# Kernel tuning notes

Measured on AMD Instinct MI355X. Metric: run time of the kernel, lower is better.

## Reference

```python
import jax, jax.numpy as jnp
import numpy as np

N, M, NNZ, N_C, D = 4096, 4096, 262144, 4, 128
ADD_RATIO, TEMP = 0.1, 0.5


def setup_inputs() -> dict:
    key = jax.random.key(0)
    ks = jax.random.split(key, 6)
    X = jax.random.normal(ks[0], (N, D), dtype=jnp.float32)
    V = jax.random.randint(ks[1], (NNZ,), 0, N)
    E = jax.random.randint(ks[2], (NNZ,), 0, M)
    # incidence matrix consistent with the (V, E) pairs
    H = jnp.zeros((N, M), jnp.float32).at[V, E].set(1.0)
    incident_mask_prob = jax.random.uniform(ks[3], (N, M), jnp.float32, 1e-4, 1.0 - 1e-4)
    cos_weight = jax.random.normal(ks[4], (N_C, D), dtype=jnp.float32)
    eps = jax.random.uniform(ks[5], (N, M), jnp.float32, 1e-6, 1.0 - 1e-6)
    return {"X": X, "H": H, "V": V, "E": E,
            "incident_mask_prob": incident_mask_prob,
            "cos_weight": cos_weight, "eps": eps}


def _l2norm(x):
    # F.normalize(p=2, dim=-1): x / max(||x||, 1e-12)
    return x / jnp.maximum(jnp.linalg.norm(x, axis=-1, keepdims=True), 1e-12)


def reference(X, H, V, E, incident_mask_prob, cos_weight, eps):
    # scatter-mean of node embeddings into edge embeddings: eX [M, D]
    counts = jax.ops.segment_sum(jnp.ones((NNZ,), X.dtype), E, num_segments=M)
    eX = jax.ops.segment_sum(X[V], E, num_segments=M) / jnp.maximum(counts, 1.0)[:, None]

    node_fc = _l2norm(X[:, None, :] * cos_weight[None])   # [N, C, D]
    edge_fc = _l2norm(eX[:, None, :] * cos_weight[None])  # [M, C, D]
    # mean over C of per-channel cosine sims -> S [N, M]
    S = jnp.einsum('ncd,mcd->nm', node_fc, edge_fc) / N_C
    S = S.at[V, E].set(-1e30)  # mask existing incidences

    num_add = max(1, int(ADD_RATIO * NNZ))
    _, idx = jax.lax.top_k(S.reshape(-1), num_add)
    row = idx // M
    col = idx % M
    delta_H = jnp.zeros_like(H).at[row, col].set(1.0)
    enriched_H = H + delta_H

    # gumbel-sigmoid with straight-through estimator
    logit = (jnp.log(eps) - jnp.log(1.0 - eps)
             + jnp.log(incident_mask_prob + 1e-8)
             - jnp.log(1.0 - incident_mask_prob + 1e-8))
    soft = jax.nn.sigmoid(logit / TEMP)
    hard = (soft > 0.5).astype(soft.dtype)
    incident_mask = hard - jax.lax.stop_gradient(soft) + soft
    return enriched_H * incident_mask
```

## Files before the change

### kernel.cpp

```cpp
#include <hip/hip_runtime.h>

#define N_NODES 4096
#define M_EDGES 4096
#define NNZ_K   262144
#define NCH     4
#define DIM     128
#define KDIM    512
#define NM      (N_NODES * M_EDGES)
#define NUM_ADD 26214
#define NCB     2048
#define NFB     32768
#define CAP     262144
#define CAP2    65536

#define EXD_OFF   0ull
#define AFC_OFF   4194304ull
#define BFC_OFF   8388608ull
#define BKT_OFF   12582912ull
#define CVAL_OFF  13631488ull
#define CIDX_OFF  15728640ull
#define CIDX2_OFF 16777216ull
#define CNT_OFF   17039360ull
#define OFFS_OFF  17055744ull
#define CUR_OFF   17072132ull
#define HIST_OFF  17088516ull
#define FHIST_OFF 17096708ull
#define SCL_OFF   17227784ull
#define ZERO_BYTES (17227848ull - CNT_OFF)
#define NINV_OFF  17227904ull
#define EINV_OFF  17358976ull

typedef short bf16x8 __attribute__((ext_vector_type(8)));
typedef float f32x4  __attribute__((ext_vector_type(4)));

#define GLOAD_LDS16(gsrc, ldst)                                                 \
    __builtin_amdgcn_global_load_lds(                                           \
        (const __attribute__((address_space(1))) void*)(gsrc),                  \
        (__attribute__((address_space(3))) void*)(ldst), 16, 0, 0)

__device__ __forceinline__ int bin_c(float s) {
    int b = (int)floorf((s + 1.0f) * 1024.0f);
    return min(max(b, 0), NCB - 1);
}

__device__ __forceinline__ int fbin_of(double v, int bstar) {
    double lo = (double)(bstar - 12) * (2.0 / 2048.0) - 1.0;
    double wd = (28.0 * (2.0 / 2048.0)) / (double)NFB;
    int f = (int)floor((v - lo) / wd);
    return min(max(f, 0), NFB - 1);
}

__device__ __forceinline__ float hard_mask(float p, float e) {
    float logit = logf(e) - logf(1.0f - e) + logf(p + 1e-8f) - logf(1.0f - p + 1e-8f);
    float soft  = 1.0f / (1.0f + expf(-2.0f * logit));
    return (soft > 0.5f) ? 1.0f : 0.0f;
}

__device__ __forceinline__ unsigned short to_bf16_rtne(float f) {
    unsigned int b = __float_as_uint(f);
    b += 0x7FFFu + ((b >> 16) & 1u);
    return (unsigned short)(b >> 16);
}

__global__ void k_count(const int* __restrict__ E, int* __restrict__ cnt) {
    int k = blockIdx.x * 256 + threadIdx.x;
    if (k < NNZ_K) atomicAdd(&cnt[E[k]], 1);
}

__global__ __launch_bounds__(256) void k_scan(const int* __restrict__ cnt, int* __restrict__ offs) {
    __shared__ int part[256];
    int t = threadIdx.x;
    int loc[16]; int s = 0;
    for (int j = 0; j < 16; ++j) { loc[j] = cnt[t * 16 + j]; s += loc[j]; }
    part[t] = s;
    __syncthreads();
    if (t == 0) { int acc = 0; for (int i = 0; i < 256; ++i) { int v = part[i]; part[i] = acc; acc += v; } }
    __syncthreads();
    int acc = part[t];
    for (int j = 0; j < 16; ++j) { offs[t * 16 + j] = acc; acc += loc[j]; }
    if (t == 255) offs[4096] = acc;
}

__global__ void k_fill(const int* __restrict__ E, const int* __restrict__ offs,
                       int* __restrict__ cur, int* __restrict__ bkt) {
    int k = blockIdx.x * 256 + threadIdx.x;
    if (k < NNZ_K) {
        int e = E[k];
        int pos = atomicAdd(&cur[e], 1);
        bkt[offs[e] + pos] = k;
    }
}

__global__ __launch_bounds__(128) void k_edge_mean(
        const int* __restrict__ Vv, const int* __restrict__ cnt,
        const int* __restrict__ offs, const int* __restrict__ bkt,
        const float* __restrict__ X, double* __restrict__ eXd) {
    __shared__ int sk[1024];
    __shared__ int sv[1024];
    int m = blockIdx.x;
    int c = cnt[m]; if (c > 1024) c = 1024;
    int off = offs[m];
    for (int t = threadIdx.x; t < c; t += 128) sk[t] = bkt[off + t];
    __syncthreads();
    for (int t = threadIdx.x; t < c; t += 128) {
        int key = sk[t]; int r = 0;
        for (int j = 0; j < c; ++j) r += (sk[j] < key);
        sv[r] = Vv[key];
    }
    __syncthreads();
    int d = threadIdx.x;
    double s = 0.0;
    for (int j = 0; j < c; ++j) s += (double)X[sv[j] * DIM + d];
    eXd[m * DIM + d] = s / (double)(c > 1 ? c : 1);
}

template <typename T>
__global__ __launch_bounds__(128) void k_fc(const T* __restrict__ in,
                                            const float* __restrict__ w,
                                            unsigned short* __restrict__ out,
                                            double* __restrict__ dinv) {
    __shared__ double red[128];
    int n = blockIdx.x, d = threadIdx.x;
    double x = (double)in[n * DIM + d];
    for (int c = 0; c < NCH; ++c) {
        double v = x * (double)w[c * DIM + d];
        red[d] = v * v;
        __syncthreads();
        for (int s = 64; s > 0; s >>= 1) { if (d < s) red[d] += red[d + s]; __syncthreads(); }
        double denom = fmax(sqrt(red[0]), 1e-12);
        __syncthreads();
        out[n * KDIM + c * DIM + d] = to_bf16_rtne((float)(v / denom));
        if (d == 0) dinv[n * NCH + c] = 1.0 / denom;
    }
}

__global__ __launch_bounds__(256) void k_gemm_mfma(const unsigned short* __restrict__ A,
                                                   const unsigned short* __restrict__ B,
                                                   float* __restrict__ S) {
    __shared__ short As[128][32];
    __shared__ short Bs[128][32];
    int tid = threadIdx.x;
    int row0 = blockIdx.y * 128, col0 = blockIdx.x * 128;
    int w = tid >> 6, l = tid & 63;
    int wr = (w >> 1) * 64, wc = (w & 1) * 64;
    f32x4 acc[4][4] = {};
    int lrow = l >> 2, lcol = (l & 3) * 8;
    int rb0 = (w * 2 + 0) * 16, rb1 = (w * 2 + 1) * 16;
    const unsigned short* sA0 = A + (size_t)(row0 + rb0 + lrow) * KDIM + lcol;
    const unsigned short* sA1 = A + (size_t)(row0 + rb1 + lrow) * KDIM + lcol;
    const unsigned short* sB0 = B + (size_t)(col0 + rb0 + lrow) * KDIM + lcol;
    const unsigned short* sB1 = B + (size_t)(col0 + rb1 + lrow) * KDIM + lcol;
    for (int k0 = 0; k0 < KDIM; k0 += 32) {
        __syncthreads();
        GLOAD_LDS16(sA0 + k0, &As[rb0][0]);
        GLOAD_LDS16(sA1 + k0, &As[rb1][0]);
        GLOAD_LDS16(sB0 + k0, &Bs[rb0][0]);
        GLOAD_LDS16(sB1 + k0, &Bs[rb1][0]);
        __syncthreads();
        int kq = (l >> 4) * 8;
        bf16x8 af[4], bfr[4];
        #pragma unroll
        for (int m = 0; m < 4; ++m) af[m] = *(const bf16x8*)&As[wr + m * 16 + (l & 15)][kq];
        #pragma unroll
        for (int n = 0; n < 4; ++n) bfr[n] = *(const bf16x8*)&Bs[wc + n * 16 + (l & 15)][kq];
        #pragma unroll
        for (int m = 0; m < 4; ++m)
            #pragma unroll
            for (int n = 0; n < 4; ++n)
                acc[m][n] = __builtin_amdgcn_mfma_f32_16x16x32_bf16(af[m], bfr[n], acc[m][n], 0, 0, 0);
    }
    #pragma unroll
    for (int m = 0; m < 4; ++m) {
        int r = row0 + wr + m * 16 + (l >> 4) * 4;
        #pragma unroll
        for (int n = 0; n < 4; ++n) {
            int c = col0 + wc + n * 16 + (l & 15);
            #pragma unroll
            for (int j = 0; j < 4; ++j)
                S[(size_t)(r + j) * M_EDGES + c] = 0.25f * acc[m][n][j];
        }
    }
}

__global__ void k_mask(const int* __restrict__ Vv, const int* __restrict__ E,
                       float* __restrict__ S) {
    int k = blockIdx.x * 256 + threadIdx.x;
    if (k < NNZ_K) S[(size_t)Vv[k] * M_EDGES + E[k]] = -1e30f;
}

__global__ __launch_bounds__(256) void k_hist_coarse(const float4* __restrict__ S4,
                                                     int* __restrict__ hist) {
    __shared__ int h[4][NCB + 8];
    int t = threadIdx.x;
    for (int i = t; i < 4 * (NCB + 8); i += 256) ((int*)h)[i] = 0;
    __syncthreads();
    int* hc = h[t & 3];
    int stride = gridDim.x * 256;
    for (int i = blockIdx.x * 256 + t; i < NM / 4; i += stride) {
        float4 v = S4[i];
        if (v.x > -2.0f) atomicAdd(&hc[bin_c(v.x)], 1);
        if (v.y > -2.0f) atomicAdd(&hc[bin_c(v.y)], 1);
        if (v.z > -2.0f) atomicAdd(&hc[bin_c(v.z)], 1);
        if (v.w > -2.0f) atomicAdd(&hc[bin_c(v.w)], 1);
    }
    __syncthreads();
    for (int i = t; i < NCB; i += 256) {
        int s = h[0][i] + h[1][i] + h[2][i] + h[3][i];
        if (s) atomicAdd(&hist[i], s);
    }
}

__global__ __launch_bounds__(256) void k_findcut(const int* __restrict__ hist, int* __restrict__ scl) {
    __shared__ int part[256];
    __shared__ int sb;
    int t = threadIdx.x;
    int loc[8]; int s = 0;
    for (int j = 0; j < 8; ++j) { loc[j] = hist[t * 8 + j]; s += loc[j]; }
    part[t] = s;
    __syncthreads();
    if (t == 0) { int acc = 0; for (int i = 255; i >= 0; --i) { int v = part[i]; part[i] = acc; acc += v; } }
    __syncthreads();
    int run = part[t];
    for (int j = 7; j >= 0; --j) {
        int h = loc[j];
        run += h;
        if (run >= NUM_ADD && run - h < NUM_ADD) { scl[0] = t * 8 + j; sb = t * 8 + j; }
    }
    __syncthreads();
    int bstar = sb;
    int g = 0;
    for (int i = bstar + 11 + t; i < NCB; i += 256) g += hist[i];
    part[t] = g;
    __syncthreads();
    for (int st2 = 128; st2 > 0; st2 >>= 1) { if (t < st2) part[t] += part[t + st2]; __syncthreads(); }
    if (t == 0) scl[1] = part[0];
}

__global__ __launch_bounds__(256) void k_collect(const float4* __restrict__ S4,
        int* __restrict__ scl, int* __restrict__ cidx, int* __restrict__ cidx2) {
    __shared__ unsigned short buf1[4096];
    __shared__ unsigned short buf2[4096];
    __shared__ int c1, c2;
    __shared__ unsigned long long gbase;
    int t = threadIdx.x;
    if (t == 0) { c1 = 0; c2 = 0; }
    __syncthreads();
    int bstar = scl[0];
    size_t base4 = (size_t)blockIdx.x * 1024 + t;
    float4 v0 = S4[base4];
    float4 v1 = S4[base4 + 256];
    float4 v2 = S4[base4 + 512];
    float4 v3 = S4[base4 + 768];
    #define COLLECT1(sc, loc)                                                   \
        if ((sc) > -2.0f) {                                                     \
            int b = bin_c(sc);                                                  \
            if (b >= bstar + 11)      buf2[atomicAdd(&c2, 1)] = (unsigned short)(loc); \
            else if (b >= bstar - 11) buf1[atomicAdd(&c1, 1)] = (unsigned short)(loc); \
        }
    #define COLLECT4(v, q)                                                      \
        COLLECT1((v).x, (t + (q)*256) * 4 + 0) COLLECT1((v).y, (t + (q)*256) * 4 + 1) \
        COLLECT1((v).z, (t + (q)*256) * 4 + 2) COLLECT1((v).w, (t + (q)*256) * 4 + 3)
    COLLECT4(v0, 0) COLLECT4(v1, 1) COLLECT4(v2, 2) COLLECT4(v3, 3)
    #undef COLLECT4
    #undef COLLECT1
    __syncthreads();
    if (t == 0) {
        unsigned long long pack = (unsigned long long)(unsigned)c1
                                | ((unsigned long long)(unsigned)c2 << 32);
        gbase = atomicAdd((unsigned long long*)&scl[8], pack);
    }
    __syncthreads();
    int g1 = (int)(gbase & 0xffffffffull);
    int g2 = (int)(gbase >> 32);
    int gb = blockIdx.x * 4096;
    for (int j = t; j < c1; j += 256) { int g = g1 + j; if (g < CAP)  cidx[g]  = gb + buf1[j]; }
    for (int j = t; j < c2; j += 256) { int g = g2 + j; if (g < CAP2) cidx2[g] = gb + buf2[j]; }
}

__global__ void k_scatter(const int* __restrict__ Vv, const int* __restrict__ E,
                          const float* __restrict__ prob, const float* __restrict__ eps,
                          float* __restrict__ out) {
    int k = blockIdx.x * 256 + threadIdx.x;
    if (k < NNZ_K) {
        size_t idx = (size_t)Vv[k] * M_EDGES + E[k];
        out[idx] = hard_mask(prob[idx], eps[idx]);
    }
}

__global__ __launch_bounds__(256) void k_selc(const int* __restrict__ scl,
        const int* __restrict__ cidx2,
        const float* __restrict__ prob, const float* __restrict__ eps,
        float* __restrict__ out) {
    int n = scl[9]; if (n > CAP2) n = CAP2;
    for (int i = blockIdx.x * 256 + threadIdx.x; i < n; i += 256 * 128) {
        int idx = cidx2[i];
        out[idx] = hard_mask(prob[idx], eps[idx]);
    }
}

__global__ __launch_bounds__(256) void k_exact(
        const int* __restrict__ scl, const int* __restrict__ cidx, double* __restrict__ cval,
        const float* __restrict__ X, const double* __restrict__ eXd, const float* __restrict__ cw,
        const double* __restrict__ ninv, const double* __restrict__ einv) {
    int nc = scl[8]; if (nc > CAP) nc = CAP;
    int wid = (blockIdx.x * 256 + threadIdx.x) >> 6;
    int l = threadIdx.x & 63;
    int nw = gridDim.x * 4;
    double w2[NCH][2];
    #pragma unroll
    for (int c = 0; c < NCH; ++c) {
        float2 wc2 = *(const float2*)&cw[c * DIM + 2 * l];
        w2[c][0] = (double)wc2.x * (double)wc2.x;
        w2[c][1] = (double)wc2.y * (double)wc2.y;
    }
    for (int i = wid; i < nc; i += nw) {
        int idx = cidx[i];
        int n = idx >> 12, m = idx & (M_EDGES - 1);
        float2  x2 = *(const float2*)&X[n * DIM + 2 * l];
        double2 e2 = *(const double2*)&eXd[m * DIM + 2 * l];
        double p0 = (double)x2.x * e2.x;
        double p1 = (double)x2.y * e2.y;
        double dt0 = p0 * w2[0][0] + p1 * w2[0][1];
        double dt1 = p0 * w2[1][0] + p1 * w2[1][1];
        double dt2 = p0 * w2[2][0] + p1 * w2[2][1];
        double dt3 = p0 * w2[3][0] + p1 * w2[3][1];
        #pragma unroll
        for (int s = 1; s < 64; s <<= 1) {
            dt0 += __shfl_xor(dt0, s);
            dt1 += __shfl_xor(dt1, s);
            dt2 += __shfl_xor(dt2, s);
            dt3 += __shfl_xor(dt3, s);
        }
        if (l == 0) {
            const double* nv = &ninv[n * NCH];
            const double* ev = &einv[m * NCH];
            cval[i] = 0.25 * (dt0 * nv[0] * ev[0] + dt1 * nv[1] * ev[1]
                            + dt2 * nv[2] * ev[2] + dt3 * nv[3] * ev[3]);
        }
    }
}

__global__ __launch_bounds__(256) void k_fhist(const int* __restrict__ scl,
                                               const int* __restrict__ cidx,
                                               const double* __restrict__ cval,
                                               int* __restrict__ fh) {
    int nc = scl[8]; if (nc > CAP) nc = CAP;
    int bstar = scl[0];
    for (int i = blockIdx.x * 256 + threadIdx.x; i < nc; i += 256 * 256)
        atomicAdd(&fh[fbin_of(cval[i], bstar)], 1);
}

__global__ __launch_bounds__(1024) void k_ffind(const int* __restrict__ fh, int* __restrict__ scl) {
    __shared__ int part[1024];
    int T = NUM_ADD - scl[1];
    int t = threadIdx.x;
    int loc[32]; int s = 0;
    for (int j = 0; j < 32; ++j) { loc[j] = fh[t * 32 + j]; s += loc[j]; }
    part[t] = s;
    __syncthreads();
    if (t == 0) { int acc = 0; for (int i = 1023; i >= 0; --i) { int v = part[i]; part[i] = acc; acc += v; } }
    __syncthreads();
    int run = part[t];
    for (int j = 31; j >= 0; --j) {
        int h = loc[j];
        run += h;
        if (run >= T && run - h < T) { scl[4] = t * 32 + j; scl[5] = run - h; }
    }
}

__global__ __launch_bounds__(256) void k_write(
        const int* __restrict__ scl, const int* __restrict__ cidx, const double* __restrict__ cval,
        const float* __restrict__ prob, const float* __restrict__ eps,
        float* __restrict__ out) {
    int nc = scl[8]; if (nc > CAP) nc = CAP;
    int fs = scl[4], bstar = scl[0];
    for (int i = blockIdx.x * 256 + threadIdx.x; i < nc; i += 256 * 256) {
        if (fbin_of(cval[i], bstar) > fs) {
            int idx = cidx[i];
            out[idx] = hard_mask(prob[idx], eps[idx]);
        }
    }
}

__global__ __launch_bounds__(256) void k_tie(
        const int* __restrict__ scl, const int* __restrict__ cidx, const double* __restrict__ cval,
        const float* __restrict__ prob, const float* __restrict__ eps,
        float* __restrict__ out) {
    __shared__ double mv[256];
    __shared__ int    mi[256];
    __shared__ int    cnt;
    int nc = scl[8]; if (nc > CAP) nc = CAP;
    int T = NUM_ADD - scl[1];
    int fs = scl[4], G1f = scl[5], bstar = scl[0];
    int t = threadIdx.x;
    if (t == 0) cnt = 0;
    __syncthreads();
    for (int i = t; i < nc; i += 256) {
        if (fbin_of(cval[i], bstar) == fs) {
            int s = atomicAdd(&cnt, 1);
            if (s < 256) { mv[s] = cval[i]; mi[s] = cidx[i]; }
        }
    }
    __syncthreads();
    int nm = min(cnt, 256);
    for (int k = t; k < nm; k += 256) {
        double v = mv[k]; int idx = mi[k];
        int rank = G1f;
        for (int j = 0; j < nm; ++j)
            rank += (mv[j] > v || (mv[j] == v && mi[j] < idx)) ? 1 : 0;
        if (rank < T)
            out[idx] = hard_mask(prob[idx], eps[idx]);
    }
}

extern "C" void kernel_launch(void* const* d_in, const int* in_sizes, int n_in,
                              void* d_out, int out_size, void* d_ws, size_t ws_size,
                              hipStream_t stream) {
    const float* X    = (const float*)d_in[0];
    const int*   Vv   = (const int*)d_in[2];
    const int*   E    = (const int*)d_in[3];
    const float* prob = (const float*)d_in[4];
    const float* cw   = (const float*)d_in[5];
    const float* eps  = (const float*)d_in[6];
    float* out = (float*)d_out;
    char*  ws  = (char*)d_ws;

    double*         eXd   = (double*)(ws + EXD_OFF);
    unsigned short* Afc   = (unsigned short*)(ws + AFC_OFF);
    unsigned short* Bfc   = (unsigned short*)(ws + BFC_OFF);
    int*            bkt   = (int*)(ws + BKT_OFF);
    double*         cval  = (double*)(ws + CVAL_OFF);
    int*            cidx  = (int*)(ws + CIDX_OFF);
    int*            cidx2 = (int*)(ws + CIDX2_OFF);
    int*            cnt   = (int*)(ws + CNT_OFF);
    int*            offs  = (int*)(ws + OFFS_OFF);
    int*            cur   = (int*)(ws + CUR_OFF);
    int*            hist  = (int*)(ws + HIST_OFF);
    int*            fh    = (int*)(ws + FHIST_OFF);
    int*            scl   = (int*)(ws + SCL_OFF);
    double*         ninv  = (double*)(ws + NINV_OFF);
    double*         einv  = (double*)(ws + EINV_OFF);

    hipMemsetAsync(ws + CNT_OFF, 0, (size_t)ZERO_BYTES, stream);

    k_count<<<NNZ_K / 256, 256, 0, stream>>>(E, cnt);
    k_scan<<<1, 256, 0, stream>>>(cnt, offs);
    k_fill<<<NNZ_K / 256, 256, 0, stream>>>(E, offs, cur, bkt);
    k_edge_mean<<<M_EDGES, 128, 0, stream>>>(Vv, cnt, offs, bkt, X, eXd);
    k_fc<float><<<N_NODES, 128, 0, stream>>>(X, cw, Afc, ninv);
    k_fc<double><<<M_EDGES, 128, 0, stream>>>(eXd, cw, Bfc, einv);
    dim3 gg(M_EDGES / 128, N_NODES / 128);
    k_gemm_mfma<<<gg, 256, 0, stream>>>(Afc, Bfc, out);
    k_mask<<<NNZ_K / 256, 256, 0, stream>>>(Vv, E, out);
    k_hist_coarse<<<1024, 256, 0, stream>>>((const float4*)out, hist);
    k_findcut<<<1, 256, 0, stream>>>(hist, scl);
    k_collect<<<4096, 256, 0, stream>>>((const float4*)out, scl, cidx, cidx2);
    hipMemsetAsync(out, 0, (size_t)NM * sizeof(float), stream);
    k_scatter<<<NNZ_K / 256, 256, 0, stream>>>(Vv, E, prob, eps, out);
    k_selc<<<128, 256, 0, stream>>>(scl, cidx2, prob, eps, out);
    k_exact<<<1024, 256, 0, stream>>>(scl, cidx, cval, X, eXd, cw, ninv, einv);
    k_fhist<<<256, 256, 0, stream>>>(scl, cidx, cval, fh);
    k_ffind<<<1, 1024, 0, stream>>>(fh, scl);
    k_write<<<256, 256, 0, stream>>>(scl, cidx, cval, prob, eps, out);
    k_tie<<<1, 256, 0, stream>>>(scl, cidx, cval, prob, eps, out);
}
```

Measured before the change: 312.4 us.

## Zero output inside collect pass and shard candidate counters into segments

The collect kernel now writes zeros over the score tile it has just read. This replaces the separate 64 MB memset of the output and saves one full write pass over the N×M buffer. The single global atomic counter for candidate lists is split into 8 segment counters with per-segment capacity, which reduces atomic contention across 4096 blocks. The downstream kernels loop over segments. The trade-off is that per-segment capacity limits (32768 and 16384) may overflow if candidates are unevenly spread across segments, which would silently drop candidates.

```diff
diff --git a/kernel.cpp b/kernel.cpp
--- a/kernel.cpp
+++ b/kernel.cpp
@@ -10,8 +10,9 @@
 #define NUM_ADD 26214
 #define NCB     2048
 #define NFB     32768
-#define CAP     262144
-#define CAP2    65536
+#define NSEG    8
+#define CAPSEG  32768
+#define CAPSEG2 16384
 
 #define EXD_OFF   0ull
 #define AFC_OFF   4194304ull
@@ -19,16 +20,17 @@
 #define BKT_OFF   12582912ull
 #define CVAL_OFF  13631488ull
 #define CIDX_OFF  15728640ull
-#define CIDX2_OFF 16777216ull
 #define CNT_OFF   17039360ull
 #define OFFS_OFF  17055744ull
 #define CUR_OFF   17072132ull
 #define HIST_OFF  17088516ull
 #define FHIST_OFF 17096708ull
 #define SCL_OFF   17227784ull
-#define ZERO_BYTES (17227848ull - CNT_OFF)
-#define NINV_OFF  17227904ull
-#define EINV_OFF  17358976ull
+#define SEGC_OFF  17227848ull
+#define ZERO_BYTES (17227912ull - CNT_OFF)
+#define NINV_OFF  17227968ull
+#define EINV_OFF  17359040ull
+#define CIDX2_OFF 17490112ull
 
 typedef short bf16x8 __attribute__((ext_vector_type(8)));
 typedef float f32x4  __attribute__((ext_vector_type(4)));
@@ -236,8 +238,9 @@
     if (t == 0) scl[1] = part[0];
 }
 
-__global__ __launch_bounds__(256) void k_collect(const float4* __restrict__ S4,
-        int* __restrict__ scl, int* __restrict__ cidx, int* __restrict__ cidx2) {
+__global__ __launch_bounds__(256) void k_collect(float4* __restrict__ S4,
+        const int* __restrict__ scl, unsigned long long* __restrict__ segc,
+        int* __restrict__ cidx, int* __restrict__ cidx2) {
     __shared__ unsigned short buf1[4096];
     __shared__ unsigned short buf2[4096];
     __shared__ int c1, c2;
@@ -263,18 +266,23 @@
     COLLECT4(v0, 0) COLLECT4(v1, 1) COLLECT4(v2, 2) COLLECT4(v3, 3)
     #undef COLLECT4
     #undef COLLECT1
-    __syncthreads();
+    float4 z = make_float4(0.f, 0.f, 0.f, 0.f);
+    S4[base4] = z; S4[base4 + 256] = z; S4[base4 + 512] = z; S4[base4 + 768] = z;
+    __syncthreads();
+    int seg = blockIdx.x & (NSEG - 1);
     if (t == 0) {
         unsigned long long pack = (unsigned long long)(unsigned)c1
                                 | ((unsigned long long)(unsigned)c2 << 32);
-        gbase = atomicAdd((unsigned long long*)&scl[8], pack);
+        gbase = atomicAdd(&segc[seg], pack);
     }
     __syncthreads();
     int g1 = (int)(gbase & 0xffffffffull);
     int g2 = (int)(gbase >> 32);
     int gb = blockIdx.x * 4096;
-    for (int j = t; j < c1; j += 256) { int g = g1 + j; if (g < CAP)  cidx[g]  = gb + buf1[j]; }
-    for (int j = t; j < c2; j += 256) { int g = g2 + j; if (g < CAP2) cidx2[g] = gb + buf2[j]; }
+    int* ci1 = cidx  + seg * CAPSEG;
+    int* ci2 = cidx2 + seg * CAPSEG2;
+    for (int j = t; j < c1; j += 256) { int g = g1 + j; if (g < CAPSEG)  ci1[g] = gb + buf1[j]; }
+    for (int j = t; j < c2; j += 256) { int g = g2 + j; if (g < CAPSEG2) ci2[g] = gb + buf2[j]; }
 }
 
 __global__ void k_scatter(const int* __restrict__ Vv, const int* __restrict__ E,
@@ -287,22 +295,25 @@
     }
 }
 
-__global__ __launch_bounds__(256) void k_selc(const int* __restrict__ scl,
+__global__ __launch_bounds__(256) void k_selc(const unsigned long long* __restrict__ segc,
         const int* __restrict__ cidx2,
         const float* __restrict__ prob, const float* __restrict__ eps,
         float* __restrict__ out) {
-    int n = scl[9]; if (n > CAP2) n = CAP2;
-    for (int i = blockIdx.x * 256 + threadIdx.x; i < n; i += 256 * 128) {
-        int idx = cidx2[i];
-        out[idx] = hard_mask(prob[idx], eps[idx]);
+    for (int s = 0; s < NSEG; ++s) {
+        int c2 = (int)(segc[s] >> 32); if (c2 > CAPSEG2) c2 = CAPSEG2;
+        const int* ci = cidx2 + s * CAPSEG2;
+        for (int i = blockIdx.x * 256 + threadIdx.x; i < c2; i += 256 * 128) {
+            int idx = ci[i];
+            out[idx] = hard_mask(prob[idx], eps[idx]);
+        }
     }
 }
 
 __global__ __launch_bounds__(256) void k_exact(
-        const int* __restrict__ scl, const int* __restrict__ cidx, double* __restrict__ cval,
+        const unsigned long long* __restrict__ segc, const int* __restrict__ cidx,
+        double* __restrict__ cval,
         const float* __restrict__ X, const double* __restrict__ eXd, const float* __restrict__ cw,
         const double* __restrict__ ninv, const double* __restrict__ einv) {
-    int nc = scl[8]; if (nc > CAP) nc = CAP;
     int wid = (blockIdx.x * 256 + threadIdx.x) >> 6;
     int l = threadIdx.x & 63;
     int nw = gridDim.x * 4;
@@ -313,41 +324,49 @@
         w2[c][0] = (double)wc2.x * (double)wc2.x;
         w2[c][1] = (double)wc2.y * (double)wc2.y;
     }
-    for (int i = wid; i < nc; i += nw) {
-        int idx = cidx[i];
-        int n = idx >> 12, m = idx & (M_EDGES - 1);
-        float2  x2 = *(const float2*)&X[n * DIM + 2 * l];
-        double2 e2 = *(const double2*)&eXd[m * DIM + 2 * l];
-        double p0 = (double)x2.x * e2.x;
-        double p1 = (double)x2.y * e2.y;
-        double dt0 = p0 * w2[0][0] + p1 * w2[0][1];
-        double dt1 = p0 * w2[1][0] + p1 * w2[1][1];
-        double dt2 = p0 * w2[2][0] + p1 * w2[2][1];
-        double dt3 = p0 * w2[3][0] + p1 * w2[3][1];
-        #pragma unroll
-        for (int s = 1; s < 64; s <<= 1) {
-            dt0 += __shfl_xor(dt0, s);
-            dt1 += __shfl_xor(dt1, s);
-            dt2 += __shfl_xor(dt2, s);
-            dt3 += __shfl_xor(dt3, s);
-        }
-        if (l == 0) {
-            const double* nv = &ninv[n * NCH];
-            const double* ev = &einv[m * NCH];
-            cval[i] = 0.25 * (dt0 * nv[0] * ev[0] + dt1 * nv[1] * ev[1]
-                            + dt2 * nv[2] * ev[2] + dt3 * nv[3] * ev[3]);
-        }
-    }
-}
-
-__global__ __launch_bounds__(256) void k_fhist(const int* __restrict__ scl,
-                                               const int* __restrict__ cidx,
+    for (int s = 0; s < NSEG; ++s) {
+        int nc = (int)(segc[s] & 0xffffffffull); if (nc > CAPSEG) nc = CAPSEG;
+        const int* ci = cidx + s * CAPSEG;
+        double* cv = cval + s * CAPSEG;
+        for (int i = wid; i < nc; i += nw) {
+            int idx = ci[i];
+            int n = idx >> 12, m = idx & (M_EDGES - 1);
+            float2  x2 = *(const float2*)&X[n * DIM + 2 * l];
+            double2 e2 = *(const double2*)&eXd[m * DIM + 2 * l];
+            double p0 = (double)x2.x * e2.x;
+            double p1 = (double)x2.y * e2.y;
+            double dt0 = p0 * w2[0][0] + p1 * w2[0][1];
+            double dt1 = p0 * w2[1][0] + p1 * w2[1][1];
+            double dt2 = p0 * w2[2][0] + p1 * w2[2][1];
+            double dt3 = p0 * w2[3][0] + p1 * w2[3][1];
+            #pragma unroll
+            for (int sh = 1; sh < 64; sh <<= 1) {
+                dt0 += __shfl_xor(dt0, sh);
+                dt1 += __shfl_xor(dt1, sh);
+                dt2 += __shfl_xor(dt2, sh);
+                dt3 += __shfl_xor(dt3, sh);
+            }
+            if (l == 0) {
+                const double* nv = &ninv[n * NCH];
+                const double* ev = &einv[m * NCH];
+                cv[i] = 0.25 * (dt0 * nv[0] * ev[0] + dt1 * nv[1] * ev[1]
+                              + dt2 * nv[2] * ev[2] + dt3 * nv[3] * ev[3]);
+            }
+        }
+    }
+}
+
+__global__ __launch_bounds__(256) void k_fhist(const unsigned long long* __restrict__ segc,
                                                const double* __restrict__ cval,
+                                               const int* __restrict__ scl,
                                                int* __restrict__ fh) {
-    int nc = scl[8]; if (nc > CAP) nc = CAP;
     int bstar = scl[0];
-    for (int i = blockIdx.x * 256 + threadIdx.x; i < nc; i += 256 * 256)
-        atomicAdd(&fh[fbin_of(cval[i], bstar)], 1);
+    for (int s = 0; s < NSEG; ++s) {
+        int nc = (int)(segc[s] & 0xffffffffull); if (nc > CAPSEG) nc = CAPSEG;
+        const double* cv = cval + s * CAPSEG;
+        for (int i = blockIdx.x * 256 + threadIdx.x; i < nc; i += 256 * 256)
+            atomicAdd(&fh[fbin_of(cv[i], bstar)], 1);
+    }
 }
 
 __global__ __launch_bounds__(1024) void k_ffind(const int* __restrict__ fh, int* __restrict__ scl) {
@@ -369,36 +388,46 @@
 }
 
 __global__ __launch_bounds__(256) void k_write(
-        const int* __restrict__ scl, const int* __restrict__ cidx, const double* __restrict__ cval,
+        const unsigned long long* __restrict__ segc, const int* __restrict__ cidx,
+        const double* __restrict__ cval, const int* __restrict__ scl,
         const float* __restrict__ prob, const float* __restrict__ eps,
         float* __restrict__ out) {
-    int nc = scl[8]; if (nc > CAP) nc = CAP;
     int fs = scl[4], bstar = scl[0];
-    for (int i = blockIdx.x * 256 + threadIdx.x; i < nc; i += 256 * 256) {
-        if (fbin_of(cval[i], bstar) > fs) {
-            int idx = cidx[i];
-            out[idx] = hard_mask(prob[idx], eps[idx]);
+    for (int s = 0; s < NSEG; ++s) {
+        int nc = (int)(segc[s] & 0xffffffffull); if (nc > CAPSEG) nc = CAPSEG;
+        const int* ci = cidx + s * CAPSEG;
+        const double* cv = cval + s * CAPSEG;
+        for (int i = blockIdx.x * 256 + threadIdx.x; i < nc; i += 256 * 256) {
+            if (fbin_of(cv[i], bstar) > fs) {
+                int idx = ci[i];
+                out[idx] = hard_mask(prob[idx], eps[idx]);
+            }
         }
     }
 }
 
 __global__ __launch_bounds__(256) void k_tie(
-        const int* __restrict__ scl, const int* __restrict__ cidx, const double* __restrict__ cval,
+        const unsigned long long* __restrict__ segc, const int* __restrict__ cidx,
+        const double* __restrict__ cval, const int* __restrict__ scl,
         const float* __restrict__ prob, const float* __restrict__ eps,
         float* __restrict__ out) {
     __shared__ double mv[256];
     __shared__ int    mi[256];
     __shared__ int    cnt;
-    int nc = scl[8]; if (nc > CAP) nc = CAP;
     int T = NUM_ADD - scl[1];
     int fs = scl[4], G1f = scl[5], bstar = scl[0];
     int t = threadIdx.x;
     if (t == 0) cnt = 0;
     __syncthreads();
-    for (int i = t; i < nc; i += 256) {
-        if (fbin_of(cval[i], bstar) == fs) {
-            int s = atomicAdd(&cnt, 1);
-            if (s < 256) { mv[s] = cval[i]; mi[s] = cidx[i]; }
+    for (int s = 0; s < NSEG; ++s) {
+        int nc = (int)(segc[s] & 0xffffffffull); if (nc > CAPSEG) nc = CAPSEG;
+        const double* cv = cval + s * CAPSEG;
+        const int* ci = cidx + s * CAPSEG;
+        for (int i = t; i < nc; i += 256) {
+            if (fbin_of(cv[i], bstar) == fs) {
+                int sl = atomicAdd(&cnt, 1);
+                if (sl < 256) { mv[sl] = cv[i]; mi[sl] = ci[i]; }
+            }
         }
     }
     __syncthreads();
@@ -425,21 +454,22 @@
     float* out = (float*)d_out;
     char*  ws  = (char*)d_ws;
 
-    double*         eXd   = (double*)(ws + EXD_OFF);
-    unsigned short* Afc   = (unsigned short*)(ws + AFC_OFF);
-    unsigned short* Bfc   = (unsigned short*)(ws + BFC_OFF);
-    int*            bkt   = (int*)(ws + BKT_OFF);
-    double*         cval  = (double*)(ws + CVAL_OFF);
-    int*            cidx  = (int*)(ws + CIDX_OFF);
-    int*            cidx2 = (int*)(ws + CIDX2_OFF);
-    int*            cnt   = (int*)(ws + CNT_OFF);
-    int*            offs  = (int*)(ws + OFFS_OFF);
-    int*            cur   = (int*)(ws + CUR_OFF);
-    int*            hist  = (int*)(ws + HIST_OFF);
-    int*            fh    = (int*)(ws + FHIST_OFF);
-    int*            scl   = (int*)(ws + SCL_OFF);
-    double*         ninv  = (double*)(ws + NINV_OFF);
-    double*         einv  = (double*)(ws + EINV_OFF);
+    double*             eXd   = (double*)(ws + EXD_OFF);
+    unsigned short*     Afc   = (unsigned short*)(ws + AFC_OFF);
+    unsigned short*     Bfc   = (unsigned short*)(ws + BFC_OFF);
+    int*                bkt   = (int*)(ws + BKT_OFF);
+    double*             cval  = (double*)(ws + CVAL_OFF);
+    int*                cidx  = (int*)(ws + CIDX_OFF);
+    int*                cidx2 = (int*)(ws + CIDX2_OFF);
+    int*                cnt   = (int*)(ws + CNT_OFF);
+    int*                offs  = (int*)(ws + OFFS_OFF);
+    int*                cur   = (int*)(ws + CUR_OFF);
+    int*                hist  = (int*)(ws + HIST_OFF);
+    int*                fh    = (int*)(ws + FHIST_OFF);
+    int*                scl   = (int*)(ws + SCL_OFF);
+    unsigned long long* segc  = (unsigned long long*)(ws + SEGC_OFF);
+    double*             ninv  = (double*)(ws + NINV_OFF);
+    double*             einv  = (double*)(ws + EINV_OFF);
 
     hipMemsetAsync(ws + CNT_OFF, 0, (size_t)ZERO_BYTES, stream);
 
@@ -454,13 +484,12 @@
     k_mask<<<NNZ_K / 256, 256, 0, stream>>>(Vv, E, out);
     k_hist_coarse<<<1024, 256, 0, stream>>>((const float4*)out, hist);
     k_findcut<<<1, 256, 0, stream>>>(hist, scl);
-    k_collect<<<4096, 256, 0, stream>>>((const float4*)out, scl, cidx, cidx2);
-    hipMemsetAsync(out, 0, (size_t)NM * sizeof(float), stream);
+    k_collect<<<4096, 256, 0, stream>>>((float4*)out, scl, segc, cidx, cidx2);
     k_scatter<<<NNZ_K / 256, 256, 0, stream>>>(Vv, E, prob, eps, out);
-    k_selc<<<128, 256, 0, stream>>>(scl, cidx2, prob, eps, out);
-    k_exact<<<1024, 256, 0, stream>>>(scl, cidx, cval, X, eXd, cw, ninv, einv);
-    k_fhist<<<256, 256, 0, stream>>>(scl, cidx, cval, fh);
+    k_selc<<<128, 256, 0, stream>>>(segc, cidx2, prob, eps, out);
+    k_exact<<<1024, 256, 0, stream>>>(segc, cidx, cval, X, eXd, cw, ninv, einv);
+    k_fhist<<<256, 256, 0, stream>>>(segc, cval, scl, fh);
     k_ffind<<<1, 1024, 0, stream>>>(fh, scl);
-    k_write<<<256, 256, 0, stream>>>(scl, cidx, cval, prob, eps, out);
-    k_tie<<<1, 256, 0, stream>>>(scl, cidx, cval, prob, eps, out);
-}
+    k_write<<<256, 256, 0, stream>>>(segc, cidx, cval, scl, prob, eps, out);
+    k_tie<<<1, 256, 0, stream>>>(segc, cidx, cval, scl, prob, eps, out);
+}
```

Measured after the change: 315.4 us. No clear change (+1.0%).
